# Kernel optimization log

Measured on AMD Instinct MI355X. Metric: run time of the kernel, lower is better.

Reference implementation:

```python
import jax, jax.numpy as jnp
import numpy as np

# SuperposedExpert: K parallel TT-factorized FFN paths + holographic routing.
# d_model=1024 factorized as [32,32]; d_ff=4096 as [64,64]; tt_ranks=[1,16,1] (r0/r2 squeezed).
K, D_MODEL, D_FF, RANK = 4, 1024, 4096, 16
IN1, IN2 = 32, 32          # factorize_for_tt(d_model)
F1, F2 = 64, 64            # factorize_for_tt(d_ff)
TEMP = 1.0                 # routing_temperature


def setup_inputs() -> dict:
    key = jax.random.key(0)
    ks = jax.random.split(key, 8)
    s = 0.05
    tokens = jax.random.normal(ks[0], (2048, D_MODEL), dtype=jnp.float32)
    # TT cores for ffn1: d_model -> d_ff  (input_dims [32,32], output_dims [64,64])
    ffn1_core1 = jax.random.normal(ks[1], (K, IN1, F1, RANK), dtype=jnp.float32) * s
    ffn1_core2 = jax.random.normal(ks[2], (K, RANK, IN2, F2), dtype=jnp.float32) * s
    # TT cores for ffn2: d_ff -> d_model (input_dims [64,64], output_dims [32,32])
    ffn2_core1 = jax.random.normal(ks[3], (K, F1, IN1, RANK), dtype=jnp.float32) * s
    ffn2_core2 = jax.random.normal(ks[4], (K, RANK, F2, IN2), dtype=jnp.float32) * s
    # Holographic routing params (hd_dim == d_model -> identity HD projection)
    pb = jax.random.normal(ks[5], (K, D_MODEL), dtype=jnp.float32)
    path_bases = pb / jnp.linalg.norm(pb, axis=-1, keepdims=True)  # orthogonal-ish init
    path_weights = jax.random.normal(ks[6], (K, D_MODEL), dtype=jnp.float32) * s
    return {
        'tokens': tokens,
        'ffn1_core1': ffn1_core1, 'ffn1_core2': ffn1_core2,
        'ffn2_core1': ffn2_core1, 'ffn2_core2': ffn2_core2,
        'path_bases': path_bases, 'path_weights': path_weights,
    }


def reference(tokens, ffn1_core1, ffn1_core2, ffn2_core1, ffn2_core2,
              path_bases, path_weights):
    N = tokens.shape[0]
    # ---- K superposed TT-FFN paths ----
    x3 = tokens.reshape(N, IN1, IN2)  # [n, a, b]
    # TT matmul 1: y[x,y] = sum_{a,b,r} G1[a,x,r] G2[r,b,y] x[a,b]
    h = jnp.einsum('nab,kaxr,krby->knxy', x3, ffn1_core1, ffn1_core2)
    h = jax.nn.gelu(h.reshape(K, N, D_FF))  # quantum_activation stand-in
    h3 = h.reshape(K, N, F1, F2)
    y = jnp.einsum('knab,kaxr,krby->knxy', h3, ffn2_core1, ffn2_core2)
    y = y.reshape(K, N, D_MODEL)  # per-path outputs
    # ---- Holographic HD routing (hd_dim == d_model: identity projection) ----
    logits = jnp.einsum('nd,kd->nk', tokens, path_bases) / TEMP
    gates = jax.nn.softmax(logits, axis=-1)  # [n, k]
    # Collapse superposition: per-path elementwise HD modulation + gated sum
    out = jnp.einsum('knd,kd,nk->nd', y, 1.0 + path_weights, gates)
    return out
```

## Files before the change

### kernel.cpp

```cpp
#include <hip/hip_runtime.h>
#include <stdint.h>

#define GAS __attribute__((address_space(1)))
#define LAS __attribute__((address_space(3)))

typedef __attribute__((ext_vector_type(8))) short short8;
typedef __attribute__((ext_vector_type(16))) float f32x16;
typedef __attribute__((ext_vector_type(4))) float f32x4;

static constexpr int N_TOK = 2048;
static constexpr int DM    = 1024;
static constexpr int DF    = 4096;
static constexpr int KP    = 4;

__device__ inline unsigned short f2bf(float f) {
  union { float f; uint32_t u; } v; v.f = f;
  uint32_t u = v.u;
  u += 0x7FFFu + ((u >> 16) & 1u);
  return (unsigned short)(u >> 16);
}

__device__ inline uint32_t pk_bf(float lo, float hi) {
  union { float f; uint32_t u; } a, b; a.f = lo; b.f = hi;
  uint32_t ul = a.u + 0x7FFFu + ((a.u >> 16) & 1u);
  uint32_t uh = b.u + 0x7FFFu + ((b.u >> 16) & 1u);
  return (ul >> 16) | (uh & 0xFFFF0000u);
}

__device__ inline float gelu_gate(float v, float g) {
  float t0 = v * v;
  float u  = v * __builtin_fmaf(t0, -0.10294456f, -2.3022539f);
  float e  = __builtin_amdgcn_exp2f(u);
  float r  = __builtin_amdgcn_rcpf(1.0f + e);
  return v * g * r;
}

__device__ inline void gld16(const void* g, void* l) {
  __builtin_amdgcn_global_load_lds((const GAS void*)g, (LAS void*)l, 16, 0, 0);
}

__global__ __launch_bounds__(256) void setup_kernel(
    const float* __restrict__ tokens, const float* __restrict__ pb,
    const float* __restrict__ c11, const float* __restrict__ c12,
    const float* __restrict__ c21, const float* __restrict__ c22,
    float* __restrict__ gates, unsigned short* __restrict__ xb,
    unsigned short* __restrict__ w1t, unsigned short* __restrict__ w2t) {
  __shared__ __align__(16) float sh[17472];
  const int blk = blockIdx.x;
  const int t = threadIdx.x;
  if (blk < 1024) {
    const int k = blk >> 8, x = (blk >> 2) & 63, y0 = (blk & 3) * 16;
    float* s1  = sh;
    float* s2T = sh + 512;
    if (t < 128) {
      int a = t >> 2, rq = (t & 3) * 4;
      *(float4*)(s1 + a * 16 + rq) =
          *(const float4*)(c11 + (((size_t)(k * 32 + a)) * 64 + x) * 16 + rq);
    }
#pragma unroll
    for (int j = 0; j < 8; ++j) {
      int i = t + j * 256;
      int rb = i >> 2, yy0 = (i & 3) * 4;
      float4 v = *(const float4*)(c12 + (size_t)(k * 16) * 2048 + (size_t)rb * 64 + y0 + yy0);
      s2T[(yy0 + 0) * 524 + rb] = v.x;
      s2T[(yy0 + 1) * 524 + rb] = v.y;
      s2T[(yy0 + 2) * 524 + rb] = v.z;
      s2T[(yy0 + 3) * 524 + rb] = v.w;
    }
    __syncthreads();
    const int a = t >> 3, b0 = (t & 7) * 4;
    float4 s1q[4];
#pragma unroll
    for (int q = 0; q < 4; ++q) s1q[q] = *(const float4*)(s1 + a * 16 + q * 4);
    const float* a0s = (const float*)s1q;
    for (int y = 0; y < 16; ++y) {
      const float* s2y = s2T + y * 524;
      float4 acc = {0.f, 0.f, 0.f, 0.f};
#pragma unroll
      for (int r = 0; r < 16; ++r) {
        float cv = a0s[r];
        float4 bv = *(const float4*)(s2y + r * 32 + b0);
        acc.x = __builtin_fmaf(cv, bv.x, acc.x);
        acc.y = __builtin_fmaf(cv, bv.y, acc.y);
        acc.z = __builtin_fmaf(cv, bv.z, acc.z);
        acc.w = __builtin_fmaf(cv, bv.w, acc.w);
      }
      ushort4 o; o.x = f2bf(acc.x); o.y = f2bf(acc.y); o.z = f2bf(acc.z); o.w = f2bf(acc.w);
      *(ushort4*)(w1t + ((size_t)k * DF + x * 64 + y0 + y) * DM + t * 4) = o;
    }
  } else if (blk < 1280) {
    const int bb = blk - 1024;
    const int k = bb >> 6, x = (bb >> 1) & 31, y0 = (bb & 1) * 16;
    float* s1  = sh;
    float* s2T = sh + 1024;
    {
      int a = t >> 2, rq = (t & 3) * 4;
      *(float4*)(s1 + a * 16 + rq) =
          *(const float4*)(c21 + (((size_t)(k * 64 + a)) * 32 + x) * 16 + rq);
    }
#pragma unroll
    for (int j = 0; j < 16; ++j) {
      int i = t + j * 256;
      int rb = i >> 2, yy0 = (i & 3) * 4;
      float4 v = *(const float4*)(c22 + (size_t)(k * 16) * 2048 + (size_t)rb * 32 + y0 + yy0);
      s2T[(yy0 + 0) * 1028 + rb] = v.x;
      s2T[(yy0 + 1) * 1028 + rb] = v.y;
      s2T[(yy0 + 2) * 1028 + rb] = v.z;
      s2T[(yy0 + 3) * 1028 + rb] = v.w;
    }
    __syncthreads();
    const int b0 = (t & 15) * 4;
#pragma unroll
    for (int jj = 0; jj < 4; ++jj) {
      const int a = (t >> 4) + jj * 16;
      float4 s1q[4];
#pragma unroll
      for (int q = 0; q < 4; ++q) s1q[q] = *(const float4*)(s1 + a * 16 + q * 4);
      const float* a0s = (const float*)s1q;
      for (int y = 0; y < 16; ++y) {
        const float* s2y = s2T + y * 1028;
        float4 acc = {0.f, 0.f, 0.f, 0.f};
#pragma unroll
        for (int r = 0; r < 16; ++r) {
          float cv = a0s[r];
          float4 bv = *(const float4*)(s2y + r * 64 + b0);
          acc.x = __builtin_fmaf(cv, bv.x, acc.x);
          acc.y = __builtin_fmaf(cv, bv.y, acc.y);
          acc.z = __builtin_fmaf(cv, bv.z, acc.z);
          acc.w = __builtin_fmaf(cv, bv.w, acc.w);
        }
        ushort4 o; o.x = f2bf(acc.x); o.y = f2bf(acc.y); o.z = f2bf(acc.z); o.w = f2bf(acc.w);
        *(ushort4*)(w2t + ((size_t)k * DM + x * 32 + y0 + y) * DF + t * 4 + jj * 1024) = o;
      }
    }
  } else {
    const int wave = t >> 6, lane = t & 63;
    const int n = (blk - 1280) * 4 + wave;
    float s0 = 0.f, s1v = 0.f, s2v = 0.f, s3v = 0.f;
    const float4* tr = (const float4*)(tokens + (size_t)n * DM);
#pragma unroll
    for (int j = 0; j < 4; ++j) {
      int idx = j * 64 + lane;
      float4 tv = tr[idx];
      ushort4 b;
      b.x = f2bf(tv.x); b.y = f2bf(tv.y); b.z = f2bf(tv.z); b.w = f2bf(tv.w);
      *(ushort4*)(xb + (size_t)n * DM + idx * 4) = b;
      float4 q;
      q = ((const float4*)(pb + 0 * DM))[idx]; s0  += tv.x*q.x + tv.y*q.y + tv.z*q.z + tv.w*q.w;
      q = ((const float4*)(pb + 1 * DM))[idx]; s1v += tv.x*q.x + tv.y*q.y + tv.z*q.z + tv.w*q.w;
      q = ((const float4*)(pb + 2 * DM))[idx]; s2v += tv.x*q.x + tv.y*q.y + tv.z*q.z + tv.w*q.w;
      q = ((const float4*)(pb + 3 * DM))[idx]; s3v += tv.x*q.x + tv.y*q.y + tv.z*q.z + tv.w*q.w;
    }
#pragma unroll
    for (int off = 32; off > 0; off >>= 1) {
      s0  += __shfl_xor(s0, off);
      s1v += __shfl_xor(s1v, off);
      s2v += __shfl_xor(s2v, off);
      s3v += __shfl_xor(s3v, off);
    }
    if (lane == 0) {
      float m = fmaxf(fmaxf(s0, s1v), fmaxf(s2v, s3v));
      float e0 = __expf(s0 - m), e1 = __expf(s1v - m), e2 = __expf(s2v - m), e3 = __expf(s3v - m);
      float inv = 1.0f / (e0 + e1 + e2 + e3);
      float4 g; g.x = e0 * inv; g.y = e1 * inv; g.z = e2 * inv; g.w = e3 * inv;
      *(float4*)(gates + n * 4) = g;
    }
  }
}

#define PH_SYNC(V) do { \
    asm volatile("s_waitcnt vmcnt(" #V ")" ::: "memory"); \
    __builtin_amdgcn_s_barrier(); \
    __builtin_amdgcn_sched_barrier(0); \
  } while (0)

#define G1_TILE(KT, BO, WO, V0, V1, V2) do { \
    const int kn_ = ((KT) + 1) * 64; \
    const bool st_ = (KT) < 15; \
     \
    PH_SYNC(V0); \
    if (st_) { const unsigned short* s_ = Wg + (size_t)srow * DM + kn_ + lch * 8; \
      gld16(s_, smem + (WO) + t * 16); gld16(s_ + 64 * DM, smem + (WO) + 8192 + t * 16); } \
    _Pragma("unroll") for (int fi = 0; fi < 4; ++fi) \
      _Pragma("unroll") for (int s = 0; s < 2; ++s) \
        af[fi][s] = *(const short8*)(smem + (BO) + aRowB + fi * 2048 + (cxor16 ^ (s * 64) ^ (fi * 32))); \
    _Pragma("unroll") for (int ti = 0; ti < 2; ++ti) \
      _Pragma("unroll") for (int s = 0; s < 2; ++s) \
        bf0[ti][s] = *(const short8*)(smem + (BO) + xRowB + ti * 2048 + (cxor16 ^ (s * 64) ^ wnx64 ^ (ti * 32))); \
    __builtin_amdgcn_s_setprio(1); \
    _Pragma("unroll") for (int fi = 0; fi < 4; ++fi) \
      _Pragma("unroll") for (int ti = 0; ti < 2; ++ti) { \
        acc[0][0][fi][ti] = __builtin_amdgcn_mfma_f32_16x16x32_bf16(af[fi][0], bf0[ti][0], acc[0][0][fi][ti], 0, 0, 0); \
        acc[0][0][fi][ti] = __builtin_amdgcn_mfma_f32_16x16x32_bf16(af[fi][1], bf0[ti][1], acc[0][0][fi][ti], 0, 0, 0); } \
    __builtin_amdgcn_s_setprio(0); \
     \
    PH_SYNC(V1); \
    if (st_) { const unsigned short* s_ = Xg + (size_t)srow * DM + kn_ + lch * 8; \
      gld16(s_, smem + (WO) + 32768 + t * 16); gld16(s_ + 64 * DM, smem + (WO) + 32768 + 8192 + t * 16); } \
    _Pragma("unroll") for (int ti = 0; ti < 2; ++ti) \
      _Pragma("unroll") for (int s = 0; s < 2; ++s) \
        bf1[ti][s] = *(const short8*)(smem + (BO) + xRowB + 16384 + ti * 2048 + (cxor16 ^ (s * 64) ^ wnx64 ^ (ti * 32))); \
    __builtin_amdgcn_s_setprio(1); \
    _Pragma("unroll") for (int fi = 0; fi < 4; ++fi) \
      _Pragma("unroll") for (int ti = 0; ti < 2; ++ti) { \
        acc[0][1][fi][ti] = __builtin_amdgcn_mfma_f32_16x16x32_bf16(af[fi][0], bf1[ti][0], acc[0][1][fi][ti], 0, 0, 0); \
        acc[0][1][fi][ti] = __builtin_amdgcn_mfma_f32_16x16x32_bf16(af[fi][1], bf1[ti][1], acc[0][1][fi][ti], 0, 0, 0); } \
    __builtin_amdgcn_s_setprio(0); \
     \
    PH_SYNC(V2); \
    if (st_) { const unsigned short* s_ = Xg + (size_t)(128 + srow) * DM + kn_ + lch * 8; \
      gld16(s_, smem + (WO) + 32768 + 16384 + t * 16); gld16(s_ + 64 * DM, smem + (WO) + 32768 + 16384 + 8192 + t * 16); } \
    _Pragma("unroll") for (int fi = 0; fi < 4; ++fi) \
      _Pragma("unroll") for (int s = 0; s < 2; ++s) \
        af[fi][s] = *(const short8*)(smem + (BO) + aRowB + 16384 + fi * 2048 + (cxor16 ^ (s * 64) ^ (fi * 32))); \
    __builtin_amdgcn_s_setprio(1); \
    _Pragma("unroll") for (int fi = 0; fi < 4; ++fi) \
      _Pragma("unroll") for (int ti = 0; ti < 2; ++ti) { \
        acc[1][1][fi][ti] = __builtin_amdgcn_mfma_f32_16x16x32_bf16(af[fi][0], bf1[ti][0], acc[1][1][fi][ti], 0, 0, 0); \
        acc[1][1][fi][ti] = __builtin_amdgcn_mfma_f32_16x16x32_bf16(af[fi][1], bf1[ti][1], acc[1][1][fi][ti], 0, 0, 0); } \
    __builtin_amdgcn_s_setprio(0); \
     \
    if (st_) { const unsigned short* s_ = Wg + (size_t)(128 + srow) * DM + kn_ + lch * 8; \
      gld16(s_, smem + (WO) + 16384 + t * 16); gld16(s_ + 64 * DM, smem + (WO) + 16384 + 8192 + t * 16); } \
    __builtin_amdgcn_s_setprio(1); \
    _Pragma("unroll") for (int fi = 0; fi < 4; ++fi) \
      _Pragma("unroll") for (int ti = 0; ti < 2; ++ti) { \
        acc[1][0][fi][ti] = __builtin_amdgcn_mfma_f32_16x16x32_bf16(af[fi][0], bf0[ti][0], acc[1][0][fi][ti], 0, 0, 0); \
        acc[1][0][fi][ti] = __builtin_amdgcn_mfma_f32_16x16x32_bf16(af[fi][1], bf0[ti][1], acc[1][0][fi][ti], 0, 0, 0); } \
    __builtin_amdgcn_s_setprio(0); \
  } while (0)

__global__ __launch_bounds__(512, 1) void gemm1(
    const unsigned short* __restrict__ xb, const unsigned short* __restrict__ w1t,
    const float* __restrict__ gates, unsigned short* __restrict__ hg) {
  __shared__ __align__(16) char smem[131072];
  const int t = threadIdx.x, lane = t & 63, wv = t >> 6;
  const int wm = wv >> 2, wn = wv & 3;
  const int m0 = blockIdx.x * 256;
  const int f0 = blockIdx.y * 256;
  const int kp = blockIdx.z;
  const unsigned short* __restrict__ Wg = w1t + (size_t)kp * DF * DM + (size_t)f0 * DM;
  const unsigned short* __restrict__ Xg = xb + (size_t)m0 * DM;

  const int srow = t >> 3;
  const int lch  = (t & 7) ^ (srow & 7) ^ (srow >> 3);
  const int l15 = lane & 15, kg = lane >> 4;
  const int cxor16 = (kg ^ (lane & 7) ^ (l15 >> 3)) * 16;
  const int wnx64  = (wn & 1) * 64;
  const int aRowB  = (wm * 64 + l15) * 128;
  const int xRowB  = 32768 + (wn * 32 + l15) * 128;

  f32x4 acc[2][2][4][2] = {};
  short8 af[4][2], bf0[2][2], bf1[2][2];

  {
    const unsigned short* sw = Wg + (size_t)srow * DM + lch * 8;
    const unsigned short* sx = Xg + (size_t)srow * DM + lch * 8;
    gld16(sw,            smem + t * 16);
    gld16(sw + 64 * DM,  smem + 8192 + t * 16);
    gld16(sx,            smem + 32768 + t * 16);
    gld16(sx + 64 * DM,  smem + 32768 + 8192 + t * 16);
    gld16(sx + 128 * DM, smem + 32768 + 16384 + t * 16);
    gld16(sx + 192 * DM, smem + 32768 + 16384 + 8192 + t * 16);
    gld16(sw + 128 * DM, smem + 16384 + t * 16);
    gld16(sw + 192 * DM, smem + 16384 + 8192 + t * 16);
  }

#pragma unroll 1
  for (int kt = 0; kt < 14; kt += 2) {
    G1_TILE(kt,     0,     65536, 4, 4, 4);
    G1_TILE(kt + 1, 65536, 0,     4, 4, 4);
  }
  G1_TILE(14, 0,     65536, 4, 4, 4);
  G1_TILE(15, 65536, 0,     4, 2, 0);

  unsigned short* __restrict__ H = hg + (size_t)kp * N_TOK * DF;
#pragma unroll
  for (int cB = 0; cB < 2; ++cB)
#pragma unroll
    for (int ti = 0; ti < 2; ++ti) {
      const int tok = m0 + cB * 128 + wn * 32 + ti * 16 + l15;
      const float g = gates[tok * 4 + kp];
      unsigned short* hrow = H + (size_t)tok * DF + f0 + wm * 64 + kg * 4;
#pragma unroll
      for (int rA = 0; rA < 2; ++rA)
#pragma unroll
        for (int fi = 0; fi < 4; ++fi) {
          f32x4 v = acc[rA][cB][fi][ti];
          float r0 = gelu_gate(v.x, g);
          float r1 = gelu_gate(v.y, g);
          float r2 = gelu_gate(v.z, g);
          float r3 = gelu_gate(v.w, g);
          uint2 p; p.x = pk_bf(r0, r1); p.y = pk_bf(r2, r3);
          *(uint2*)(hrow + rA * 128 + fi * 16) = p;
        }
    }
}

__global__ __launch_bounds__(256) void gemm2(
    const unsigned short* __restrict__ hg, const unsigned short* __restrict__ w2t,
    const float* __restrict__ pw, float* __restrict__ part) {
  __shared__ __align__(16) unsigned short As[128 * 64];
  __shared__ __align__(16) unsigned short Bs[128 * 64];
  const int t = threadIdx.x, lane = t & 63, wv = t >> 6;
  const int m0 = blockIdx.x * 128;
  const int n0 = blockIdx.y * 128;
  const int kp = blockIdx.z;
  const unsigned short* A = hg + (size_t)kp * N_TOK * DF;
  const unsigned short* B = w2t + (size_t)kp * DM * DF;
  f32x16 acc[2][2] = {};
  const int srow = t >> 3;
  const int sbase = ((t & 7) ^ (srow & 7) ^ (srow >> 3)) * 8;
  const int wdrow = (wv >> 1) * 64, wtcol = (wv & 1) * 64;
  const int l31 = lane & 31, khalf = lane >> 5;
  const int rsw = (l31 & 7) ^ (l31 >> 3);
  char* AsB = (char*)As;
  char* BsB = (char*)Bs;
  for (int k0 = 0; k0 < DF; k0 += 64) {
#pragma unroll
    for (int i = 0; i < 4; ++i) {
      int row = i * 32 + srow;
      int sc = sbase ^ ((i & 1) * 32);
      gld16(A + (size_t)(m0 + row) * DF + k0 + sc, AsB + i * 4096 + t * 16);
      gld16(B + (size_t)(n0 + row) * DF + k0 + sc, BsB + i * 4096 + t * 16);
    }
    __syncthreads();
#pragma unroll
    for (int s = 0; s < 4; ++s) {
      const int lc = s * 2 + khalf;
      short8 a[2], b[2];
#pragma unroll
      for (int mi = 0; mi < 2; ++mi) {
        const int pc = ((lc ^ rsw ^ (mi * 4)) & 7) * 8;
        a[mi] = *(const short8*)(Bs + (wdrow + mi * 32 + l31) * 64 + pc);
      }
#pragma unroll
      for (int ni = 0; ni < 2; ++ni) {
        const int pc = ((lc ^ rsw ^ (ni * 4)) & 7) * 8;
        b[ni] = *(const short8*)(As + (wtcol + ni * 32 + l31) * 64 + pc);
      }
#pragma unroll
      for (int mi = 0; mi < 2; ++mi)
#pragma unroll
        for (int ni = 0; ni < 2; ++ni)
          acc[mi][ni] = __builtin_amdgcn_mfma_f32_32x32x16_bf16(a[mi], b[ni], acc[mi][ni], 0, 0, 0);
    }
    __syncthreads();
  }
  float* P = part + (size_t)kp * N_TOK * DM;
  const int rbase = 4 * khalf;
  float4 pwv[2][4];
#pragma unroll
  for (int mi = 0; mi < 2; ++mi)
#pragma unroll
    for (int gq = 0; gq < 4; ++gq) {
      float4 w = *(const float4*)(pw + kp * DM + n0 + wdrow + mi * 32 + rbase + 8 * gq);
      pwv[mi][gq].x = 1.0f + w.x; pwv[mi][gq].y = 1.0f + w.y;
      pwv[mi][gq].z = 1.0f + w.z; pwv[mi][gq].w = 1.0f + w.w;
    }
#pragma unroll
  for (int ni = 0; ni < 2; ++ni) {
    int tok = m0 + wtcol + ni * 32 + l31;
    float* prow = P + (size_t)tok * DM + n0;
#pragma unroll
    for (int mi = 0; mi < 2; ++mi) {
      int dbase = wdrow + mi * 32 + rbase;
#pragma unroll
      for (int gq = 0; gq < 4; ++gq) {
        float4 o;
        o.x = pwv[mi][gq].x * acc[mi][ni][4 * gq + 0];
        o.y = pwv[mi][gq].y * acc[mi][ni][4 * gq + 1];
        o.z = pwv[mi][gq].z * acc[mi][ni][4 * gq + 2];
        o.w = pwv[mi][gq].w * acc[mi][ni][4 * gq + 3];
        *(float4*)(prow + dbase + 8 * gq) = o;
      }
    }
  }
}

__global__ __launch_bounds__(256) void reduce_k(
    const float* __restrict__ part, float* __restrict__ out) {
  const size_t i = ((size_t)blockIdx.x * 256 + threadIdx.x) * 4;
  const size_t S = (size_t)N_TOK * DM;
  float4 a = *(const float4*)(part + i);
  float4 b = *(const float4*)(part + S + i);
  float4 c = *(const float4*)(part + 2 * S + i);
  float4 d = *(const float4*)(part + 3 * S + i);
  float4 r;
  r.x = a.x + b.x + c.x + d.x;
  r.y = a.y + b.y + c.y + d.y;
  r.z = a.z + b.z + c.z + d.z;
  r.w = a.w + b.w + c.w + d.w;
  *(float4*)(out + i) = r;
}

extern "C" void kernel_launch(void* const* d_in, const int* in_sizes, int n_in,
                              void* d_out, int out_size, void* d_ws, size_t ws_size,
                              hipStream_t stream) {
  const float* tokens = (const float*)d_in[0];
  const float* f1c1   = (const float*)d_in[1];
  const float* f1c2   = (const float*)d_in[2];
  const float* f2c1   = (const float*)d_in[3];
  const float* f2c2   = (const float*)d_in[4];
  const float* pb     = (const float*)d_in[5];
  const float* pw     = (const float*)d_in[6];
  float* out = (float*)d_out;

  char* ws = (char*)d_ws;
  unsigned short* xb  = (unsigned short*)(ws);
  unsigned short* w1t = (unsigned short*)(ws + (4ull  << 20));
  float*          part = (float*)(ws + (4ull << 20));
  unsigned short* w2t = (unsigned short*)(ws + (36ull << 20));
  unsigned short* hg  = (unsigned short*)(ws + (68ull << 20));
  float*          gates = (float*)(ws + (132ull << 20));

  hipLaunchKernelGGL(setup_kernel, dim3(1792), dim3(256), 0, stream,
                     tokens, pb, f1c1, f1c2, f2c1, f2c2, gates, xb, w1t, w2t);
  hipLaunchKernelGGL(gemm1, dim3(8, 16, KP), dim3(512), 0, stream, xb, w1t, gates, hg);
  hipLaunchKernelGGL(gemm2, dim3(16, 8, KP), dim3(256), 0, stream, hg, w2t, pw, part);
  hipLaunchKernelGGL(reduce_k, dim3(2048), dim3(256), 0, stream, part, out);
}
```

Measured before the change: 258.1 us.

## Rewrite gemm2 as double-buffered 256x128 tile with phased prefetch and 16x16 MFMA

Replaces the simple single-buffered gemm2 loop with a 512-thread, 256x128-tile kernel modeled on gemm1. It double-buffers 96KB of LDS and interleaves the next tile's global-to-LDS loads with MFMA phases, using PH_SYNC barriers and s_setprio. The aim is to hide global load latency and raise data reuse per block. The cost is 256 blocks instead of 512, fewer waves per CU, and tighter barrier correctness requirements.

```diff
diff --git a/kernel.cpp b/kernel.cpp
--- a/kernel.cpp
+++ b/kernel.cpp
@@ -297,85 +297,132 @@
     }
 }
 
-__global__ __launch_bounds__(256) void gemm2(
+#define G2_TILE(KT, BO, WO, V0, V1, V2) do { \
+    const int kn_ = ((KT) + 1) * 64; \
+    const bool st_ = (KT) < 63; \
+     \
+    PH_SYNC(V0); \
+    if (st_) gld16(Wg + (size_t)srow * DF + kn_ + lch * 8, smem + (WO) + t * 16); \
+    _Pragma("unroll") for (int fi = 0; fi < 2; ++fi) \
+      _Pragma("unroll") for (int s = 0; s < 2; ++s) \
+        af[fi][s] = *(const short8*)(smem + (BO) + awRowB + fi * 2048 + (cxor16 ^ awx ^ (fi * 32) ^ (s * 64))); \
+    _Pragma("unroll") for (int ti = 0; ti < 2; ++ti) \
+      _Pragma("unroll") for (int s = 0; s < 2; ++s) \
+        bf0[ti][s] = *(const short8*)(smem + (BO) + xRowB + ti * 2048 + (cxor16 ^ wnx64 ^ (ti * 32) ^ (s * 64))); \
+    __builtin_amdgcn_s_setprio(1); \
+    _Pragma("unroll") for (int fi = 0; fi < 2; ++fi) \
+      _Pragma("unroll") for (int ti = 0; ti < 2; ++ti) { \
+        acc[0][0][fi][ti] = __builtin_amdgcn_mfma_f32_16x16x32_bf16(af[fi][0], bf0[ti][0], acc[0][0][fi][ti], 0, 0, 0); \
+        acc[0][0][fi][ti] = __builtin_amdgcn_mfma_f32_16x16x32_bf16(af[fi][1], bf0[ti][1], acc[0][0][fi][ti], 0, 0, 0); } \
+    __builtin_amdgcn_s_setprio(0); \
+     \
+    PH_SYNC(V1); \
+    if (st_) { const unsigned short* s_ = Xg + (size_t)srow * DF + kn_ + lch * 8; \
+      gld16(s_, smem + (WO) + 16384 + t * 16); gld16(s_ + 64 * DF, smem + (WO) + 16384 + 8192 + t * 16); } \
+    _Pragma("unroll") for (int ti = 0; ti < 2; ++ti) \
+      _Pragma("unroll") for (int s = 0; s < 2; ++s) \
+        bf1[ti][s] = *(const short8*)(smem + (BO) + xRowB + 16384 + ti * 2048 + (cxor16 ^ wnx64 ^ (ti * 32) ^ (s * 64))); \
+    __builtin_amdgcn_s_setprio(1); \
+    _Pragma("unroll") for (int fi = 0; fi < 2; ++fi) \
+      _Pragma("unroll") for (int ti = 0; ti < 2; ++ti) { \
+        acc[0][1][fi][ti] = __builtin_amdgcn_mfma_f32_16x16x32_bf16(af[fi][0], bf1[ti][0], acc[0][1][fi][ti], 0, 0, 0); \
+        acc[0][1][fi][ti] = __builtin_amdgcn_mfma_f32_16x16x32_bf16(af[fi][1], bf1[ti][1], acc[0][1][fi][ti], 0, 0, 0); } \
+    __builtin_amdgcn_s_setprio(0); \
+     \
+    PH_SYNC(V2); \
+    if (st_) { const unsigned short* s_ = Xg + (size_t)(128 + srow) * DF + kn_ + lch * 8; \
+      gld16(s_, smem + (WO) + 32768 + t * 16); gld16(s_ + 64 * DF, smem + (WO) + 32768 + 8192 + t * 16); } \
+    _Pragma("unroll") for (int fi = 0; fi < 2; ++fi) \
+      _Pragma("unroll") for (int s = 0; s < 2; ++s) \
+        af[fi][s] = *(const short8*)(smem + (BO) + awRowB + 8192 + fi * 2048 + (cxor16 ^ awx ^ (fi * 32) ^ (s * 64))); \
+    __builtin_amdgcn_s_setprio(1); \
+    _Pragma("unroll") for (int fi = 0; fi < 2; ++fi) \
+      _Pragma("unroll") for (int ti = 0; ti < 2; ++ti) { \
+        acc[1][1][fi][ti] = __builtin_amdgcn_mfma_f32_16x16x32_bf16(af[fi][0], bf1[ti][0], acc[1][1][fi][ti], 0, 0, 0); \
+        acc[1][1][fi][ti] = __builtin_amdgcn_mfma_f32_16x16x32_bf16(af[fi][1], bf1[ti][1], acc[1][1][fi][ti], 0, 0, 0); } \
+    __builtin_amdgcn_s_setprio(0); \
+     \
+    if (st_) gld16(Wg + (size_t)(64 + srow) * DF + kn_ + lch * 8, smem + (WO) + 8192 + t * 16); \
+    __builtin_amdgcn_s_setprio(1); \
+    _Pragma("unroll") for (int fi = 0; fi < 2; ++fi) \
+      _Pragma("unroll") for (int ti = 0; ti < 2; ++ti) { \
+        acc[1][0][fi][ti] = __builtin_amdgcn_mfma_f32_16x16x32_bf16(af[fi][0], bf0[ti][0], acc[1][0][fi][ti], 0, 0, 0); \
+        acc[1][0][fi][ti] = __builtin_amdgcn_mfma_f32_16x16x32_bf16(af[fi][1], bf0[ti][1], acc[1][0][fi][ti], 0, 0, 0); } \
+    __builtin_amdgcn_s_setprio(0); \
+  } while (0)
+
+__global__ __launch_bounds__(512, 1) void gemm2(
     const unsigned short* __restrict__ hg, const unsigned short* __restrict__ w2t,
     const float* __restrict__ pw, float* __restrict__ part) {
-  __shared__ __align__(16) unsigned short As[128 * 64];
-  __shared__ __align__(16) unsigned short Bs[128 * 64];
+  __shared__ __align__(16) char smem[98304];
   const int t = threadIdx.x, lane = t & 63, wv = t >> 6;
-  const int m0 = blockIdx.x * 128;
+  const int wm = wv >> 2, wn = wv & 3;
+  const int m0 = blockIdx.x * 256;
   const int n0 = blockIdx.y * 128;
   const int kp = blockIdx.z;
-  const unsigned short* A = hg + (size_t)kp * N_TOK * DF;
-  const unsigned short* B = w2t + (size_t)kp * DM * DF;
-  f32x16 acc[2][2] = {};
+  const unsigned short* __restrict__ Wg = w2t + (size_t)kp * DM * DF + (size_t)n0 * DF;
+  const unsigned short* __restrict__ Xg = hg + (size_t)kp * N_TOK * DF + (size_t)m0 * DF;
+
   const int srow = t >> 3;
-  const int sbase = ((t & 7) ^ (srow & 7) ^ (srow >> 3)) * 8;
-  const int wdrow = (wv >> 1) * 64, wtcol = (wv & 1) * 64;
-  const int l31 = lane & 31, khalf = lane >> 5;
-  const int rsw = (l31 & 7) ^ (l31 >> 3);
-  char* AsB = (char*)As;
-  char* BsB = (char*)Bs;
-  for (int k0 = 0; k0 < DF; k0 += 64) {
-#pragma unroll
-    for (int i = 0; i < 4; ++i) {
-      int row = i * 32 + srow;
-      int sc = sbase ^ ((i & 1) * 32);
-      gld16(A + (size_t)(m0 + row) * DF + k0 + sc, AsB + i * 4096 + t * 16);
-      gld16(B + (size_t)(n0 + row) * DF + k0 + sc, BsB + i * 4096 + t * 16);
-    }
-    __syncthreads();
-#pragma unroll
-    for (int s = 0; s < 4; ++s) {
-      const int lc = s * 2 + khalf;
-      short8 a[2], b[2];
-#pragma unroll
-      for (int mi = 0; mi < 2; ++mi) {
-        const int pc = ((lc ^ rsw ^ (mi * 4)) & 7) * 8;
-        a[mi] = *(const short8*)(Bs + (wdrow + mi * 32 + l31) * 64 + pc);
-      }
-#pragma unroll
-      for (int ni = 0; ni < 2; ++ni) {
-        const int pc = ((lc ^ rsw ^ (ni * 4)) & 7) * 8;
-        b[ni] = *(const short8*)(As + (wtcol + ni * 32 + l31) * 64 + pc);
-      }
-#pragma unroll
-      for (int mi = 0; mi < 2; ++mi)
-#pragma unroll
-        for (int ni = 0; ni < 2; ++ni)
-          acc[mi][ni] = __builtin_amdgcn_mfma_f32_32x32x16_bf16(a[mi], b[ni], acc[mi][ni], 0, 0, 0);
-    }
-    __syncthreads();
+  const int lch  = (t & 7) ^ (srow & 7) ^ (srow >> 3);
+  const int l15 = lane & 15, kg = lane >> 4;
+  const int cxor16 = (kg ^ (lane & 7) ^ (l15 >> 3)) * 16;
+  const int wnx64  = (wn & 1) * 64;
+  const int awx    = wm * 64;
+  const int awRowB = (wm * 32 + l15) * 128;
+  const int xRowB  = 16384 + (wn * 32 + l15) * 128;
+
+  f32x4 acc[2][2][2][2] = {};
+  short8 af[2][2], bf0[2][2], bf1[2][2];
+
+  {
+    const unsigned short* sw = Wg + (size_t)srow * DF + lch * 8;
+    const unsigned short* sx = Xg + (size_t)srow * DF + lch * 8;
+    gld16(sw,            smem + t * 16);
+    gld16(sx,            smem + 16384 + t * 16);
+    gld16(sx + 64 * DF,  smem + 16384 + 8192 + t * 16);
+    gld16(sx + 128 * DF, smem + 32768 + t * 16);
+    gld16(sx + 192 * DF, smem + 32768 + 8192 + t * 16);
+    gld16(sw + 64 * DF,  smem + 8192 + t * 16);
   }
-  float* P = part + (size_t)kp * N_TOK * DM;
-  const int rbase = 4 * khalf;
-  float4 pwv[2][4];
-#pragma unroll
-  for (int mi = 0; mi < 2; ++mi)
-#pragma unroll
-    for (int gq = 0; gq < 4; ++gq) {
-      float4 w = *(const float4*)(pw + kp * DM + n0 + wdrow + mi * 32 + rbase + 8 * gq);
-      pwv[mi][gq].x = 1.0f + w.x; pwv[mi][gq].y = 1.0f + w.y;
-      pwv[mi][gq].z = 1.0f + w.z; pwv[mi][gq].w = 1.0f + w.w;
-    }
-#pragma unroll
-  for (int ni = 0; ni < 2; ++ni) {
-    int tok = m0 + wtcol + ni * 32 + l31;
-    float* prow = P + (size_t)tok * DM + n0;
-#pragma unroll
-    for (int mi = 0; mi < 2; ++mi) {
-      int dbase = wdrow + mi * 32 + rbase;
-#pragma unroll
-      for (int gq = 0; gq < 4; ++gq) {
-        float4 o;
-        o.x = pwv[mi][gq].x * acc[mi][ni][4 * gq + 0];
-        o.y = pwv[mi][gq].y * acc[mi][ni][4 * gq + 1];
-        o.z = pwv[mi][gq].z * acc[mi][ni][4 * gq + 2];
-        o.w = pwv[mi][gq].w * acc[mi][ni][4 * gq + 3];
-        *(float4*)(prow + dbase + 8 * gq) = o;
-      }
-    }
+
+#pragma unroll 1
+  for (int kt = 0; kt < 62; kt += 2) {
+    G2_TILE(kt,     0,     49152, 3, 2, 3);
+    G2_TILE(kt + 1, 49152, 0,     3, 2, 3);
   }
+  G2_TILE(62, 0,     49152, 3, 2, 3);
+  G2_TILE(63, 49152, 0,     3, 1, 0);
+
+  float* __restrict__ P = part + (size_t)kp * N_TOK * DM;
+  float4 pwv[2][2];
+#pragma unroll
+  for (int rA = 0; rA < 2; ++rA)
+#pragma unroll
+    for (int fi = 0; fi < 2; ++fi) {
+      float4 w = *(const float4*)(pw + kp * DM + n0 + rA * 64 + wm * 32 + fi * 16 + kg * 4);
+      pwv[rA][fi].x = 1.0f + w.x; pwv[rA][fi].y = 1.0f + w.y;
+      pwv[rA][fi].z = 1.0f + w.z; pwv[rA][fi].w = 1.0f + w.w;
+    }
+#pragma unroll
+  for (int cB = 0; cB < 2; ++cB)
+#pragma unroll
+    for (int ti = 0; ti < 2; ++ti) {
+      const int tok = m0 + cB * 128 + wn * 32 + ti * 16 + l15;
+      float* prow = P + (size_t)tok * DM + n0 + wm * 32 + kg * 4;
+#pragma unroll
+      for (int rA = 0; rA < 2; ++rA)
+#pragma unroll
+        for (int fi = 0; fi < 2; ++fi) {
+          f32x4 v = acc[rA][cB][fi][ti];
+          float4 o;
+          o.x = pwv[rA][fi].x * v.x;
+          o.y = pwv[rA][fi].y * v.y;
+          o.z = pwv[rA][fi].z * v.z;
+          o.w = pwv[rA][fi].w * v.w;
+          *(float4*)(prow + rA * 64 + fi * 16) = o;
+        }
+    }
 }
 
 __global__ __launch_bounds__(256) void reduce_k(
@@ -417,6 +464,6 @@
   hipLaunchKernelGGL(setup_kernel, dim3(1792), dim3(256), 0, stream,
                      tokens, pb, f1c1, f1c2, f2c1, f2c2, gates, xb, w1t, w2t);
   hipLaunchKernelGGL(gemm1, dim3(8, 16, KP), dim3(512), 0, stream, xb, w1t, gates, hg);
-  hipLaunchKernelGGL(gemm2, dim3(16, 8, KP), dim3(256), 0, stream, hg, w2t, pw, part);
+  hipLaunchKernelGGL(gemm2, dim3(8, 8, KP), dim3(512), 0, stream, hg, w2t, pw, part);
   hipLaunchKernelGGL(reduce_k, dim3(2048), dim3(256), 0, stream, part, out);
 }
```

New measurement: 247.4 us. 4.2% less time.
